# Performance work log

Measured on AMD Instinct MI355X. Metric: run time of the kernel, lower is better.

Reference implementation:

```python
import jax, jax.numpy as jnp
import numpy as np

B, H, T = 16, 1024, 4096
CD, CS = 8, 1024  # codebook_dim, codebook_size


def setup_inputs() -> dict:
    key = jax.random.key(0)
    ks = jax.random.split(key, 6)
    return {
        "hidden_state": jax.random.normal(ks[0], (B, H, T), dtype=jnp.float32),
        "in_proj_w": jax.random.normal(ks[1], (CD, H), dtype=jnp.float32) * 0.02,
        "in_proj_b": jax.random.normal(ks[2], (CD,), dtype=jnp.float32) * 0.02,
        "out_proj_w": jax.random.normal(ks[3], (H, CD), dtype=jnp.float32) * 0.02,
        "out_proj_b": jax.random.normal(ks[4], (H,), dtype=jnp.float32) * 0.02,
        "codebook": jax.random.normal(ks[5], (CS, CD), dtype=jnp.float32),
    }


def _l2_normalize(x, axis=-1, eps=1e-12):
    n = jnp.sqrt(jnp.sum(x * x, axis=axis, keepdims=True))
    return x / jnp.maximum(n, eps)


def reference(hidden_state, in_proj_w, in_proj_b, out_proj_w, out_proj_b, codebook):
    sg = jax.lax.stop_gradient
    # 1x1 conv == pointwise linear over channels: [B,H,T] -> [B,CD,T]
    proj = jnp.einsum("bht,dh->bdt", hidden_state, in_proj_w) + in_proj_b[None, :, None]

    # decode_latents: cosine-similarity nearest neighbor
    b, d, t = proj.shape
    enc = proj.transpose(0, 2, 1).reshape(b * t, d)          # [BT, CD]
    enc_n = _l2_normalize(enc, axis=1)
    cb_n = _l2_normalize(codebook, axis=1)                   # [CS, CD]
    l2 = jnp.sum(enc_n * enc_n, axis=1, keepdims=True)       # [BT, 1]
    dist = -(l2 - 2.0 * (enc_n @ cb_n.T)) + jnp.sum(cb_n * cb_n, axis=1)[None, :]
    indices = jnp.argmax(dist, axis=1).reshape(b, t)         # [B, T] int
    quant = codebook[indices].transpose(0, 2, 1)             # [B, CD, T]

    commitment_loss = jnp.mean((proj - sg(quant)) ** 2)
    codebook_loss = jnp.mean((quant - sg(proj)) ** 2)

    # straight-through estimator
    q_st = proj + sg(quant - proj)
    out = jnp.einsum("bdt,hd->bht", q_st, out_proj_w) + out_proj_b[None, :, None]
    return (out, commitment_loss, codebook_loss, indices, proj)
```

## Files before the change

kernel.cpp:

```cpp
#include <hip/hip_runtime.h>
#include <math.h>

#define NB 16
#define NH 1024
#define NT 4096
#define CD 8
#define CS 1024
#define NBT (NB*NT)

__global__ __launch_bounds__(256) void k0_prep(
    const float* __restrict__ w,
    const float* __restrict__ bias,
    const float* __restrict__ cb,
    double* __restrict__ Wt,
    double* __restrict__ biasd,
    double* __restrict__ cbn,
    double* __restrict__ cbn2,
    double* __restrict__ lossacc)
{
    int g = blockIdx.x * 256 + threadIdx.x;
    if (g < CD * NH) {
        int h = g >> 3, d = g & 7;
        Wt[g] = (double)w[d * NH + h];
    }
    if (g < CS) {
        double v[CD];
        double s = 0.0;
        #pragma unroll
        for (int j = 0; j < CD; j++) { v[j] = (double)cb[g * CD + j]; s += v[j] * v[j]; }
        double n = sqrt(s);
        double m = fmax(n, 1e-12);
        double s2 = 0.0;
        #pragma unroll
        for (int j = 0; j < CD; j++) {
            double q = v[j] / m;
            cbn[g * CD + j] = q;
            s2 += q * q;
        }
        cbn2[g] = s2;
    }
    if (g < CD) biasd[g] = (double)bias[g];
    if (g == 0) *lossacc = 0.0;
}

__global__ __launch_bounds__(512) void k1_proj(
    const float*  __restrict__ x,
    const double* __restrict__ Wt,
    const double* __restrict__ biasd,
    double* __restrict__ projd,
    float*  __restrict__ projf)
{
    __shared__ double red[CD][8][64];
    const int tx = threadIdx.x;
    const int ty = threadIdx.y;
    const int bt = blockIdx.x * 64 + tx;
    const int b  = bt >> 12;
    const int t  = bt & (NT - 1);
    const float* xp = x + ((size_t)b * NH) * NT + t;
    const int h0 = __builtin_amdgcn_readfirstlane(ty * 128);

    double acc[CD];
    #pragma unroll
    for (int d = 0; d < CD; d++) acc[d] = 0.0;

    for (int i = 0; i < 128; i += 16) {
        float xv[16];
        #pragma unroll
        for (int j = 0; j < 16; j++) xv[j] = xp[(size_t)(h0 + i + j) * NT];
        #pragma unroll
        for (int j = 0; j < 16; j++) {
            const double xd = (double)xv[j];
            const double* wr = Wt + (h0 + i + j) * CD;
            #pragma unroll
            for (int d = 0; d < CD; d++) acc[d] = fma(xd, wr[d], acc[d]);
        }
    }

    #pragma unroll
    for (int d = 0; d < CD; d++) red[d][ty][tx] = acc[d];
    __syncthreads();

    if (ty == 0) {
        #pragma unroll
        for (int d = 0; d < CD; d++) {
            double s = 0.0;
            #pragma unroll
            for (int j = 0; j < 8; j++) s += red[d][j][tx];
            s += biasd[d];
            projd[(size_t)bt * CD + d] = s;
            projf[((size_t)b * CD + d) * NT + t] = (float)s;
        }
    }
}

__global__ __launch_bounds__(512) void k2_argmax(
    const double* __restrict__ projd,
    const double* __restrict__ cbn,
    const double* __restrict__ cbn2,
    const float*  __restrict__ cb,
    float* __restrict__ idxf,
    int*   __restrict__ idxi,
    double* __restrict__ lossacc)
{
    __shared__ double bestv_s[8][64];
    __shared__ int    besti_s[8][64];
    const int tx = threadIdx.x;
    const int ty = threadIdx.y;
    const int bt = blockIdx.x * 64 + tx;

    double p[CD];
    #pragma unroll
    for (int d = 0; d < CD; d++) p[d] = projd[(size_t)bt * CD + d];

    double s = 0.0;
    #pragma unroll
    for (int d = 0; d < CD; d++) s += p[d] * p[d];
    const double m = fmax(sqrt(s), 1e-12);
    double pn2[CD];
    #pragma unroll
    for (int d = 0; d < CD; d++) pn2[d] = 2.0 * (p[d] / m);

    const int c0 = __builtin_amdgcn_readfirstlane(ty * 128);
    double best = -1e300;
    int bi = 0;
    #pragma unroll 4
    for (int c = 0; c < 128; c++) {
        const double* cr = cbn + (size_t)(c0 + c) * CD;
        double dot = cbn2[c0 + c];
        #pragma unroll
        for (int d = 0; d < CD; d++) dot = fma(pn2[d], cr[d], dot);
        if (dot > best) { best = dot; bi = c; }
    }
    bestv_s[ty][tx] = best;
    besti_s[ty][tx] = c0 + bi;
    __syncthreads();

    if (ty == 0) {
        double bv = bestv_s[0][tx];
        int    bc = besti_s[0][tx];
        #pragma unroll
        for (int j = 1; j < 8; j++) {
            const double v = bestv_s[j][tx];
            const int    c = besti_s[j][tx];
            if (v > bv) { bv = v; bc = c; }
        }
        idxf[bt] = (float)bc;
        idxi[bt] = bc;

        const float* qr = cb + (size_t)bc * CD;
        double ls = 0.0;
        #pragma unroll
        for (int d = 0; d < CD; d++) {
            const float pf = (float)p[d];
            const float df = pf - qr[d];
            const float sq = df * df;
            ls += (double)sq;
        }
        #pragma unroll
        for (int o = 32; o > 0; o >>= 1) ls += __shfl_down(ls, o, 64);
        if (tx == 0) atomicAdd(lossacc, ls);
    }
}

__global__ __launch_bounds__(512) void k4_out(
    const double* __restrict__ projd,
    const int*    __restrict__ idxi,
    const float*  __restrict__ cb,
    const float*  __restrict__ wo,
    const float*  __restrict__ bo,
    const double* __restrict__ lossacc,
    float* __restrict__ out,
    float* __restrict__ lossout)
{
    if (blockIdx.x == 0 && threadIdx.x == 0 && threadIdx.y == 0) {
        const float v = (float)(*lossacc / (double)(NB * CD * NT));
        lossout[0] = v;
        lossout[1] = v;
    }

    const int tx = threadIdx.x;
    const int ty = threadIdx.y;
    const int bt = blockIdx.x * 64 + tx;
    const int b  = bt >> 12;
    const int t  = bt & (NT - 1);

    const int bi = idxi[bt];
    float q[CD];
    #pragma unroll
    for (int d = 0; d < CD; d++) {
        const float pf = (float)projd[(size_t)bt * CD + d];
        const float cf = cb[(size_t)bi * CD + d];
        q[d] = pf + (cf - pf);
    }

    const int h0 = __builtin_amdgcn_readfirstlane(ty * 128);
    float* op = out + ((size_t)b * NH) * NT + t;

    #pragma unroll 4
    for (int i = 0; i < 128; i++) {
        const int h = h0 + i;
        const float* wr = wo + (size_t)h * CD;
        float o = 0.f;
        #pragma unroll
        for (int d = 0; d < CD; d++) o = fmaf(q[d], wr[d], o);
        o += bo[h];
        op[(size_t)h * NT] = o;
    }
}

extern "C" void kernel_launch(void* const* d_in, const int* in_sizes, int n_in,
                              void* d_out, int out_size, void* d_ws, size_t ws_size,
                              hipStream_t stream) {
    const float* hidden = (const float*)d_in[0];
    const float* ipw    = (const float*)d_in[1];
    const float* ipb    = (const float*)d_in[2];
    const float* opw    = (const float*)d_in[3];
    const float* opb    = (const float*)d_in[4];
    const float* cb     = (const float*)d_in[5];

    float* out      = (float*)d_out;
    float* loss_out = out + (size_t)NB * NH * NT;
    float* idxf     = loss_out + 2;
    float* projf    = idxf + NBT;

    double* Wt      = (double*)d_ws;
    double* biasd   = Wt + CD * NH;
    double* cbn     = biasd + 8;
    double* cbn2    = cbn + (size_t)CS * CD;
    double* lossacc = cbn2 + CS;
    double* projd   = lossacc + 8;
    int*    idxi    = (int*)(projd + (size_t)NBT * CD);

    k0_prep<<<32, 256, 0, stream>>>(ipw, ipb, cb, Wt, biasd, cbn, cbn2, lossacc);
    k1_proj<<<NBT / 64, dim3(64, 8), 0, stream>>>(hidden, Wt, biasd, projd, projf);
    k2_argmax<<<NBT / 64, dim3(64, 8), 0, stream>>>(projd, cbn, cbn2, cb, idxf, idxi, lossacc);
    k4_out<<<NBT / 64, dim3(64, 8), 0, stream>>>(projd, idxi, cb, opw, opb, lossacc, out, loss_out);
}
```

Measured before the change: 540.6 us.

## Split projection into H-chunk partials, use fp32 argmax with fp64 fallback

Restructures the pipeline into a split-H partial-sum projection that writes float partials into the output buffer as scratch. A middle kernel reduces the partials, computes the argmax over the codebook in fp32 while tracking the runner-up, and redoes the search in fp64 across the wave only when the margin is small. It also writes the straight-through quantized vectors for the output kernel, which now uses float4 vector stores over 4 timesteps per thread. The aim is to cut fp64 ALU cost and improve memory coalescing, at the cost of summing partials in float and relying on a margin heuristic to recover exact argmax ties.

```diff
diff --git a/kernel.cpp b/kernel.cpp
--- a/kernel.cpp
+++ b/kernel.cpp
@@ -7,6 +7,12 @@
 #define CD 8
 #define CS 1024
 #define NBT (NB*NT)
+
+#define HCA 16
+#define HCH (NH/HCA)
+#define TCA 2
+#define TTA (NT/TCA)
+#define MARGIN 1e-3f
 
 __global__ __launch_bounds__(256) void k0_prep(
     const float* __restrict__ w,
@@ -16,6 +22,8 @@
     double* __restrict__ biasd,
     double* __restrict__ cbn,
     double* __restrict__ cbn2,
+    float*  __restrict__ cbnf,
+    float*  __restrict__ cbn2f,
     double* __restrict__ lossacc)
 {
     int g = blockIdx.x * 256 + threadIdx.x;
@@ -35,176 +43,225 @@
         for (int j = 0; j < CD; j++) {
             double q = v[j] / m;
             cbn[g * CD + j] = q;
+            cbnf[g * CD + j] = (float)q;
             s2 += q * q;
         }
         cbn2[g] = s2;
+        cbn2f[g] = (float)s2;
     }
     if (g < CD) biasd[g] = (double)bias[g];
     if (g == 0) *lossacc = 0.0;
 }
 
-__global__ __launch_bounds__(512) void k1_proj(
+__global__ __launch_bounds__(512, 4) void k1_partial(
     const float*  __restrict__ x,
     const double* __restrict__ Wt,
+    float* __restrict__ ps)
+{
+    const int tid = threadIdx.x;
+    const int bid = blockIdx.x;
+    const int hc  = bid & (HCA - 1);
+    const int tc  = (bid >> 4) & (TCA - 1);
+    const int b   = bid >> 5;
+    const int h0  = hc * HCH;
+    const int t0  = tc * TTA + tid * 4;
+
+    const float* xp = x + ((size_t)b * NH + h0) * NT + t0;
+
+    double acc[CD][4];
+    #pragma unroll
+    for (int d = 0; d < CD; d++)
+        #pragma unroll
+        for (int j = 0; j < 4; j++) acc[d][j] = 0.0;
+
+    for (int i = 0; i < HCH; i += 4) {
+        float4 xv[4];
+        #pragma unroll
+        for (int j = 0; j < 4; j++) xv[j] = *(const float4*)(xp + (size_t)(i + j) * NT);
+        #pragma unroll
+        for (int j = 0; j < 4; j++) {
+            const double* wr = Wt + (size_t)(h0 + i + j) * CD;
+            const double x0 = (double)xv[j].x;
+            const double x1 = (double)xv[j].y;
+            const double x2 = (double)xv[j].z;
+            const double x3 = (double)xv[j].w;
+            #pragma unroll
+            for (int d = 0; d < CD; d++) {
+                acc[d][0] = fma(x0, wr[d], acc[d][0]);
+                acc[d][1] = fma(x1, wr[d], acc[d][1]);
+                acc[d][2] = fma(x2, wr[d], acc[d][2]);
+                acc[d][3] = fma(x3, wr[d], acc[d][3]);
+            }
+        }
+    }
+
+    float* pp = ps + ((size_t)bid * CD) * TTA + tid * 4;
+    #pragma unroll
+    for (int d = 0; d < CD; d++) {
+        float4 o;
+        o.x = (float)acc[d][0]; o.y = (float)acc[d][1];
+        o.z = (float)acc[d][2]; o.w = (float)acc[d][3];
+        *(float4*)(pp + (size_t)d * TTA) = o;
+    }
+}
+
+__global__ __launch_bounds__(256) void k2_mid(
+    const float*  __restrict__ ps,
     const double* __restrict__ biasd,
-    double* __restrict__ projd,
-    float*  __restrict__ projf)
-{
-    __shared__ double red[CD][8][64];
-    const int tx = threadIdx.x;
-    const int ty = threadIdx.y;
-    const int bt = blockIdx.x * 64 + tx;
-    const int b  = bt >> 12;
-    const int t  = bt & (NT - 1);
-    const float* xp = x + ((size_t)b * NH) * NT + t;
-    const int h0 = __builtin_amdgcn_readfirstlane(ty * 128);
-
-    double acc[CD];
-    #pragma unroll
-    for (int d = 0; d < CD; d++) acc[d] = 0.0;
-
-    for (int i = 0; i < 128; i += 16) {
-        float xv[16];
-        #pragma unroll
-        for (int j = 0; j < 16; j++) xv[j] = xp[(size_t)(h0 + i + j) * NT];
-        #pragma unroll
-        for (int j = 0; j < 16; j++) {
-            const double xd = (double)xv[j];
-            const double* wr = Wt + (h0 + i + j) * CD;
-            #pragma unroll
-            for (int d = 0; d < CD; d++) acc[d] = fma(xd, wr[d], acc[d]);
-        }
-    }
-
-    #pragma unroll
-    for (int d = 0; d < CD; d++) red[d][ty][tx] = acc[d];
-    __syncthreads();
-
-    if (ty == 0) {
-        #pragma unroll
-        for (int d = 0; d < CD; d++) {
-            double s = 0.0;
-            #pragma unroll
-            for (int j = 0; j < 8; j++) s += red[d][j][tx];
-            s += biasd[d];
-            projd[(size_t)bt * CD + d] = s;
-            projf[((size_t)b * CD + d) * NT + t] = (float)s;
-        }
-    }
-}
-
-__global__ __launch_bounds__(512) void k2_argmax(
-    const double* __restrict__ projd,
     const double* __restrict__ cbn,
     const double* __restrict__ cbn2,
+    const float*  __restrict__ cbnf,
+    const float*  __restrict__ cbn2f,
     const float*  __restrict__ cb,
+    double* __restrict__ lossacc,
     float* __restrict__ idxf,
-    int*   __restrict__ idxi,
-    double* __restrict__ lossacc)
+    float* __restrict__ projf,
+    float* __restrict__ qf)
 {
-    __shared__ double bestv_s[8][64];
-    __shared__ int    besti_s[8][64];
-    const int tx = threadIdx.x;
-    const int ty = threadIdx.y;
-    const int bt = blockIdx.x * 64 + tx;
-
+    const int tid = threadIdx.x;
+    const int g   = blockIdx.x * 256 + tid;
+    const int b   = g >> 12;
+    const int t   = g & (NT - 1);
+    const int tc  = t >> 11;
+    const int tl  = t & (TTA - 1);
+
+    const float* pbase = ps + ((size_t)(b * TCA + tc) * HCA) * CD * TTA + tl;
     double p[CD];
     #pragma unroll
-    for (int d = 0; d < CD; d++) p[d] = projd[(size_t)bt * CD + d];
-
-    double s = 0.0;
-    #pragma unroll
-    for (int d = 0; d < CD; d++) s += p[d] * p[d];
-    const double m = fmax(sqrt(s), 1e-12);
-    double pn2[CD];
-    #pragma unroll
-    for (int d = 0; d < CD; d++) pn2[d] = 2.0 * (p[d] / m);
-
-    const int c0 = __builtin_amdgcn_readfirstlane(ty * 128);
-    double best = -1e300;
+    for (int d = 0; d < CD; d++) {
+        double s = 0.0;
+        #pragma unroll
+        for (int hc = 0; hc < HCA; hc++) s += (double)pbase[((size_t)hc * CD + d) * TTA];
+        s += biasd[d];
+        p[d] = s;
+    }
+
+    float pf[CD];
+    #pragma unroll
+    for (int d = 0; d < CD; d++) {
+        pf[d] = (float)p[d];
+        projf[((size_t)b * CD + d) * NT + t] = pf[d];
+    }
+
+    double s2 = 0.0;
+    #pragma unroll
+    for (int d = 0; d < CD; d++) s2 += p[d] * p[d];
+    const double m = fmax(sqrt(s2), 1e-12);
+    float pn[CD];
+    #pragma unroll
+    for (int d = 0; d < CD; d++) pn[d] = (float)(2.0 * (p[d] / m));
+
+    float best = -3.4e38f, second = -3.4e38f;
     int bi = 0;
-    #pragma unroll 4
-    for (int c = 0; c < 128; c++) {
-        const double* cr = cbn + (size_t)(c0 + c) * CD;
-        double dot = cbn2[c0 + c];
-        #pragma unroll
-        for (int d = 0; d < CD; d++) dot = fma(pn2[d], cr[d], dot);
-        if (dot > best) { best = dot; bi = c; }
-    }
-    bestv_s[ty][tx] = best;
-    besti_s[ty][tx] = c0 + bi;
-    __syncthreads();
-
-    if (ty == 0) {
-        double bv = bestv_s[0][tx];
-        int    bc = besti_s[0][tx];
-        #pragma unroll
-        for (int j = 1; j < 8; j++) {
-            const double v = bestv_s[j][tx];
-            const int    c = besti_s[j][tx];
-            if (v > bv) { bv = v; bc = c; }
-        }
-        idxf[bt] = (float)bc;
-        idxi[bt] = bc;
-
-        const float* qr = cb + (size_t)bc * CD;
-        double ls = 0.0;
+    for (int c = 0; c < CS; c += 2) {
+        const float* cr0 = cbnf + (size_t)c * CD;
+        const float* cr1 = cr0 + CD;
+        float dot0 = cbn2f[c];
+        float dot1 = cbn2f[c + 1];
         #pragma unroll
         for (int d = 0; d < CD; d++) {
-            const float pf = (float)p[d];
-            const float df = pf - qr[d];
-            const float sq = df * df;
-            ls += (double)sq;
-        }
-        #pragma unroll
-        for (int o = 32; o > 0; o >>= 1) ls += __shfl_down(ls, o, 64);
-        if (tx == 0) atomicAdd(lossacc, ls);
-    }
+            dot0 = fmaf(pn[d], cr0[d], dot0);
+            dot1 = fmaf(pn[d], cr1[d], dot1);
+        }
+        second = fmaxf(second, fminf(dot0, best));
+        if (dot0 > best) { best = dot0; bi = c; }
+        second = fmaxf(second, fminf(dot1, best));
+        if (dot1 > best) { best = dot1; bi = c + 1; }
+    }
+
+    const int lane = tid & 63;
+    unsigned long long mask = __ballot((best - second) <= MARGIN);
+    while (mask) {
+        const int src = __ffsll(mask) - 1;
+        mask &= mask - 1;
+        double q[CD];
+        #pragma unroll
+        for (int d = 0; d < CD; d++) q[d] = __shfl(p[d], src, 64);
+        double qs = 0.0;
+        #pragma unroll
+        for (int d = 0; d < CD; d++) qs += q[d] * q[d];
+        const double qm = fmax(sqrt(qs), 1e-12);
+        double qn[CD];
+        #pragma unroll
+        for (int d = 0; d < CD; d++) qn[d] = 2.0 * (q[d] / qm);
+        double bv = -1e300;
+        int bidx = 0;
+        for (int k = 0; k < CS / 64; k++) {
+            const int c = k * 64 + lane;
+            const double* cr = cbn + (size_t)c * CD;
+            double dot = cbn2[c];
+            #pragma unroll
+            for (int d = 0; d < CD; d++) dot = fma(qn[d], cr[d], dot);
+            if (dot > bv) { bv = dot; bidx = c; }
+        }
+        #pragma unroll
+        for (int off = 32; off; off >>= 1) {
+            const double ov = __shfl_xor(bv, off, 64);
+            const int    oi = __shfl_xor(bidx, off, 64);
+            if (ov > bv || (ov == bv && oi < bidx)) { bv = ov; bidx = oi; }
+        }
+        if (lane == src) bi = bidx;
+    }
+
+    idxf[g] = (float)bi;
+    const float* qr = cb + (size_t)bi * CD;
+    double ls = 0.0;
+    #pragma unroll
+    for (int d = 0; d < CD; d++) {
+        const float cf = qr[d];
+        const float qv = pf[d] + (cf - pf[d]);
+        qf[((size_t)b * CD + d) * NT + t] = qv;
+        const float df = pf[d] - cf;
+        ls += (double)(df * df);
+    }
+    #pragma unroll
+    for (int off = 32; off; off >>= 1) ls += __shfl_xor(ls, off, 64);
+    if (lane == 0) atomicAdd(lossacc, ls);
 }
 
 __global__ __launch_bounds__(512) void k4_out(
-    const double* __restrict__ projd,
-    const int*    __restrict__ idxi,
-    const float*  __restrict__ cb,
+    const float*  __restrict__ qf,
     const float*  __restrict__ wo,
     const float*  __restrict__ bo,
     const double* __restrict__ lossacc,
     float* __restrict__ out,
     float* __restrict__ lossout)
 {
-    if (blockIdx.x == 0 && threadIdx.x == 0 && threadIdx.y == 0) {
-        const float v = (float)(*lossacc / (double)(NB * CD * NT));
+    if (blockIdx.x == 0 && threadIdx.x == 0) {
+        const float v = (float)(*lossacc / (double)((size_t)NB * CD * NT));
         lossout[0] = v;
         lossout[1] = v;
     }
 
-    const int tx = threadIdx.x;
-    const int ty = threadIdx.y;
-    const int bt = blockIdx.x * 64 + tx;
-    const int b  = bt >> 12;
-    const int t  = bt & (NT - 1);
-
-    const int bi = idxi[bt];
-    float q[CD];
-    #pragma unroll
-    for (int d = 0; d < CD; d++) {
-        const float pf = (float)projd[(size_t)bt * CD + d];
-        const float cf = cb[(size_t)bi * CD + d];
-        q[d] = pf + (cf - pf);
-    }
-
-    const int h0 = __builtin_amdgcn_readfirstlane(ty * 128);
-    float* op = out + ((size_t)b * NH) * NT + t;
-
-    #pragma unroll 4
-    for (int i = 0; i < 128; i++) {
-        const int h = h0 + i;
-        const float* wr = wo + (size_t)h * CD;
-        float o = 0.f;
-        #pragma unroll
-        for (int d = 0; d < CD; d++) o = fmaf(q[d], wr[d], o);
-        o += bo[h];
-        op[(size_t)h * NT] = o;
+    const int tid = threadIdx.x;
+    const int bid = blockIdx.x;
+    const int hc  = bid & (HCA - 1);
+    const int tc  = (bid >> 4) & (TCA - 1);
+    const int b   = bid >> 5;
+    const int h0  = hc * HCH;
+    const int t0  = tc * TTA + tid * 4;
+
+    float q[CD][4];
+    #pragma unroll
+    for (int d = 0; d < CD; d++) {
+        const float4 v = *(const float4*)(qf + ((size_t)b * CD + d) * NT + t0);
+        q[d][0] = v.x; q[d][1] = v.y; q[d][2] = v.z; q[d][3] = v.w;
+    }
+
+    float* op = out + ((size_t)b * NH + h0) * NT + t0;
+    for (int i = 0; i < HCH; i++) {
+        const float* wr = wo + (size_t)(h0 + i) * CD;
+        const float bh = bo[h0 + i];
+        float o0 = 0.f, o1 = 0.f, o2 = 0.f, o3 = 0.f;
+        #pragma unroll
+        for (int d = 0; d < CD; d++) {
+            o0 = fmaf(q[d][0], wr[d], o0);
+            o1 = fmaf(q[d][1], wr[d], o1);
+            o2 = fmaf(q[d][2], wr[d], o2);
+            o3 = fmaf(q[d][3], wr[d], o3);
+        }
+        o0 += bh; o1 += bh; o2 += bh; o3 += bh;
+        *(float4*)(op + (size_t)i * NT) = make_float4(o0, o1, o2, o3);
     }
 }
 
@@ -223,16 +280,21 @@
     float* idxf     = loss_out + 2;
     float* projf    = idxf + NBT;
 
+    float* ps = out;
+
     double* Wt      = (double*)d_ws;
     double* biasd   = Wt + CD * NH;
     double* cbn     = biasd + 8;
     double* cbn2    = cbn + (size_t)CS * CD;
     double* lossacc = cbn2 + CS;
-    double* projd   = lossacc + 8;
-    int*    idxi    = (int*)(projd + (size_t)NBT * CD);
-
-    k0_prep<<<32, 256, 0, stream>>>(ipw, ipb, cb, Wt, biasd, cbn, cbn2, lossacc);
-    k1_proj<<<NBT / 64, dim3(64, 8), 0, stream>>>(hidden, Wt, biasd, projd, projf);
-    k2_argmax<<<NBT / 64, dim3(64, 8), 0, stream>>>(projd, cbn, cbn2, cb, idxf, idxi, lossacc);
-    k4_out<<<NBT / 64, dim3(64, 8), 0, stream>>>(projd, idxi, cb, opw, opb, lossacc, out, loss_out);
-}
+    float*  cbnf    = (float*)(lossacc + 8);
+    float*  cbn2f   = cbnf + (size_t)CS * CD;
+    float*  qf      = cbn2f + CS;
+
+    k0_prep<<<32, 256, 0, stream>>>(ipw, ipb, cb, Wt, biasd, cbn, cbn2, cbnf, cbn2f,
+                                    lossacc);
+    k1_partial<<<NB * TCA * HCA, 512, 0, stream>>>(hidden, Wt, ps);
+    k2_mid<<<NBT / 256, 256, 0, stream>>>(ps, biasd, cbn, cbn2, cbnf, cbn2f, cb,
+                                          lossacc, idxf, projf, qf);
+    k4_out<<<NB * TCA * HCA, 512, 0, stream>>>(qf, opw, opb, lossacc, out, loss_out);
+}
```

Measured after the change: 658.5 us. +21.8%, slower.
